# Performance work log

Measured on AMD Instinct MI355X. Metric: run time of the kernel, lower is better.

## Reference

```python
import jax, jax.numpy as jnp
import numpy as np

B, L, D, H = 4, 1024, 1024, 16
HD = D // H
EPS = 1e-5


def _split_heads(x):
    b, l, d = x.shape
    return x.reshape(b, l, H, HD).transpose(0, 2, 1, 3)  # [B,H,L,hd]


def _combine_heads(x):
    b, h, l, hd = x.shape
    return x.transpose(0, 2, 1, 3).reshape(b, l, h * hd)


def _attention(q, k, v):
    scores = jnp.einsum('bhqd,bhkd->bhqk', q, k) / jnp.sqrt(jnp.asarray(HD, q.dtype))
    w = jax.nn.softmax(scores, axis=-1)  # dropout is identity in eval mode
    return jnp.einsum('bhqk,bhkd->bhqd', w, v)


def _layernorm(x, g, b):
    mu = jnp.mean(x, axis=-1, keepdims=True)
    var = jnp.mean(jnp.square(x - mu), axis=-1, keepdims=True)
    return (x - mu) * jax.lax.rsqrt(var + EPS) * g + b


def setup_inputs() -> dict:
    key = jax.random.key(0)
    ks = jax.random.split(key, 20)
    s = 1.0 / np.sqrt(D)
    s2 = 1.0 / np.sqrt(2 * D)
    # weights stored as (in, out): y = x @ W + b
    inp = {
        'h_b': jax.random.normal(ks[0], (B, L, D), jnp.float32),
        'h_p': jax.random.normal(ks[1], (B, L, D), jnp.float32),
        'wq': jax.random.uniform(ks[2], (D, D), jnp.float32, -s, s),
        'bq': jnp.zeros((D,), jnp.float32),
        'wk_sem': jax.random.uniform(ks[3], (D, D), jnp.float32, -s, s),
        'bk_sem': jnp.zeros((D,), jnp.float32),
        'wk_syn': jax.random.uniform(ks[4], (D, D), jnp.float32, -s, s),
        'bk_syn': jnp.zeros((D,), jnp.float32),
        'wv': jax.random.uniform(ks[5], (D, D), jnp.float32, -s, s),
        'bv': jnp.zeros((D,), jnp.float32),
        'g_sem_w': jax.random.uniform(ks[6], (2 * D, D), jnp.float32, -s2, s2),
        'g_sem_b': jnp.zeros((D,), jnp.float32),
        'g_syn_w': jax.random.uniform(ks[7], (2 * D, D), jnp.float32, -s2, s2),
        'g_syn_b': jnp.zeros((D,), jnp.float32),
        'ln_sem_g': jnp.ones((D,), jnp.float32),
        'ln_sem_b': jnp.zeros((D,), jnp.float32),
        'ln_syn_g': jnp.ones((D,), jnp.float32),
        'ln_syn_b': jnp.zeros((D,), jnp.float32),
        'fg1_w': jax.random.uniform(ks[8], (2 * D, D), jnp.float32, -s2, s2),
        'fg1_b': jnp.zeros((D,), jnp.float32),
        'fg2_w': jax.random.uniform(ks[9], (D, 1), jnp.float32, -s, s),
        'fg2_b': jnp.zeros((1,), jnp.float32),
    }
    return inp


def reference(h_b, h_p, wq, bq, wk_sem, bk_sem, wk_syn, bk_syn, wv, bv,
              g_sem_w, g_sem_b, g_syn_w, g_syn_b,
              ln_sem_g, ln_sem_b, ln_syn_g, ln_syn_b,
              fg1_w, fg1_b, fg2_w, fg2_b):
    def cross_attn(a, b, kw, kb):
        q = _split_heads(a @ wq + bq)
        k = _split_heads(b @ kw + kb)
        v = _split_heads(b @ wv + bv)
        return _combine_heads(_attention(q, k, v))

    def gate_fusion(orig, enh, gw, gb):
        gate = jax.nn.sigmoid(jnp.concatenate([orig, enh], axis=-1) @ gw + gb)
        return gate * enh + (1.0 - gate) * orig

    # semantic branch: query=h_b, kv=h_p with syntax K/V projections
    enh_b = cross_attn(h_b, h_p, wk_syn, bk_syn)
    hbp = gate_fusion(h_b, enh_b, g_sem_w, g_sem_b)
    hbp = _layernorm(hbp + h_b, ln_sem_g, ln_sem_b)

    # syntax branch: query=h_p, kv=h_b with semantic K projection (as in source)
    enh_p = cross_attn(h_p, h_b, wk_sem, bk_sem)
    hpp = gate_fusion(h_p, enh_p, g_syn_w, g_syn_b)
    hpp = _layernorm(hpp + h_p, ln_syn_g, ln_syn_b)

    cat = jnp.concatenate([hbp, hpp], axis=-1)
    fw = jax.nn.sigmoid(jax.nn.relu(cat @ fg1_w + fg1_b) @ fg2_w + fg2_b)  # [B,L,1]
    return fw * hbp + (1.0 - fw) * hpp
```

## Files before the change

kernel.cpp:

```cpp
#include <hip/hip_runtime.h>


typedef __bf16 bf16;
typedef __attribute__((ext_vector_type(4))) __bf16 bf16x4;
typedef __attribute__((ext_vector_type(8))) __bf16 bf16x8;
typedef __attribute__((ext_vector_type(4))) float f32x4;

#define MFMA16(a, b, c) __builtin_amdgcn_mfma_f32_16x16x32_bf16((a), (b), (c), 0, 0, 0)
#define EXP2(x) __builtin_amdgcn_exp2f(x)

__device__ inline void async16(const bf16* g, bf16* l) {
  __builtin_amdgcn_global_load_lds(
      (const __attribute__((address_space(1))) unsigned int*)g,
      (__attribute__((address_space(3))) unsigned int*)l, 16, 0, 0);
}

__global__ __launch_bounds__(256) void prep_k(
    const float* __restrict__ wq, const float* __restrict__ wk_sem,
    const float* __restrict__ wk_syn, const float* __restrict__ wv,
    const float* __restrict__ g_sem_w, const float* __restrict__ g_syn_w,
    const float* __restrict__ fg1_w, const float* __restrict__ h_b,
    const float* __restrict__ h_p, bf16* __restrict__ wqT,
    bf16* __restrict__ wkSemT, bf16* __restrict__ wkSynT,
    bf16* __restrict__ wvT, bf16* __restrict__ gSemT,
    bf16* __restrict__ gSynT, bf16* __restrict__ fg1T,
    bf16* __restrict__ hbb, bf16* __restrict__ hpb) {
  int blk = blockIdx.x, tid = threadIdx.x;
  if (blk >= 10240) {
    int idx = blk - 10240;
    const float* in = (idx < 2048) ? h_b : h_p;
    bf16* out = (idx < 2048) ? hbb : hpb;
    size_t base = (size_t)(idx & 2047) * 2048 + tid * 8;
    f32x4 x = *(const f32x4*)(in + base), y = *(const f32x4*)(in + base + 4);
    bf16x8 r;
#pragma unroll
    for (int j = 0; j < 4; j++) { r[j] = (bf16)x[j]; r[4 + j] = (bf16)y[j]; }
    *(bf16x8*)(out + base) = r;
    return;
  }
  __shared__ bf16 t[32][33];
  const float* in;
  bf16* out;
  int R, tile;
  if (blk < 4096) {
    int which = blk >> 10;
    tile = blk & 1023;
    R = 1024;
    in = (which == 0) ? wq : (which == 1) ? wk_sem : (which == 2) ? wk_syn : wv;
    out = (which == 0) ? wqT
          : (which == 1) ? wkSemT : (which == 2) ? wkSynT : wvT;
  } else {
    int b2 = blk - 4096;
    int which = b2 >> 11;
    tile = b2 & 2047;
    R = 2048;
    in = (which == 0) ? g_sem_w : (which == 1) ? g_syn_w : fg1_w;
    out = (which == 0) ? gSemT : (which == 1) ? gSynT : fg1T;
  }
  const int C = 1024;
  int c0 = (tile & 31) * 32, r0 = (tile >> 5) * 32;
  int tx = tid & 31, ty = tid >> 5;
#pragma unroll
  for (int i = 0; i < 32; i += 8)
    t[ty + i][tx] = (bf16)in[(size_t)(r0 + ty + i) * C + c0 + tx];
  __syncthreads();
#pragma unroll
  for (int i = 0; i < 32; i += 8)
    out[(size_t)(c0 + ty + i) * R + r0 + tx] = t[tx][ty + i];
}

__device__ inline void stage128(bf16* Ls, const bf16* src, int r0, int k0,
                                int ldk, int tid) {
#pragma unroll
  for (int i = 0; i < 2; i++) {
    int s = tid + i * 256;
    int row = s >> 2, ch = s & 3;
    async16(src + (size_t)(r0 + row) * ldk + k0 + ch * 8,
            Ls + ((size_t)(i * 256 + (tid & ~63))) * 8);
  }
}
__device__ inline void stage64(bf16* Ls, const bf16* src, int r0, int k0,
                               int ldk, int tid) {
  int row = tid >> 2, ch = tid & 3;
  async16(src + (size_t)(r0 + row) * ldk + k0 + ch * 8,
          Ls + ((size_t)(tid & ~63)) * 8);
}

__global__ __launch_bounds__(256) void proj_gemm(
    const bf16* __restrict__ hbb, const bf16* __restrict__ hpb,
    const bf16* __restrict__ wqT, const bf16* __restrict__ wkSemT,
    const bf16* __restrict__ wkSynT, const bf16* __restrict__ wvT,
    const float* __restrict__ bq, const float* __restrict__ bk_sem,
    const float* __restrict__ bk_syn, const float* __restrict__ bv,
    bf16* __restrict__ q0, bf16* __restrict__ q1, bf16* __restrict__ k0b,
    bf16* __restrict__ k1b, bf16* __restrict__ v0t, bf16* __restrict__ v1t) {
  __shared__ bf16 As[128 * 32];
  __shared__ bf16 Bs[128 * 32];
  int tid = threadIdx.x;
  int m0g = blockIdx.y * 128;
  int half = m0g >= 4096;
  int m0 = m0g & 4095;
  int n0g = blockIdx.x * 128;
  int seg = n0g >> 10, n0 = n0g & 1023;

  const bf16* A = half ? hpb : hbb;
  const bf16* Wt = (seg == 0) ? wqT
                   : (seg == 1) ? (half ? wkSynT : wkSemT) : wvT;
  const float* bias = (seg == 0) ? bq
                      : (seg == 1) ? (half ? bk_syn : bk_sem) : bv;

  int w = tid >> 6, lane = tid & 63, quad = lane >> 4, ln = lane & 15;
  int wm = (w >> 1) * 64, wn = (w & 1) * 64;

  const f32x4 z = {0.f, 0.f, 0.f, 0.f};
  f32x4 acc[4][4];
#pragma unroll
  for (int i = 0; i < 4; i++)
#pragma unroll
    for (int j = 0; j < 4; j++) acc[i][j] = z;

  for (int k0 = 0; k0 < 1024; k0 += 32) {
    __syncthreads();
    stage128(Bs, Wt, n0, k0, 1024, tid);
    stage128(As, A, m0, k0, 1024, tid);
    __syncthreads();
    bf16x8 af[4], bfv[4];
#pragma unroll
    for (int mt = 0; mt < 4; mt++)
      af[mt] = *(bf16x8*)(As + (wm + mt * 16 + ln) * 32 + quad * 8);
#pragma unroll
    for (int nt = 0; nt < 4; nt++)
      bfv[nt] = *(bf16x8*)(Bs + (wn + nt * 16 + ln) * 32 + quad * 8);
#pragma unroll
    for (int mt = 0; mt < 4; mt++)
#pragma unroll
      for (int nt = 0; nt < 4; nt++)
        acc[mt][nt] = MFMA16(af[mt], bfv[nt], acc[mt][nt]);
  }

  if (seg == 2) {
    bf16* vt = half ? v0t : v1t;
#pragma unroll
    for (int nt = 0; nt < 4; nt++) {
      int n = n0 + wn + nt * 16 + ln;
      float bvv = bias[n];
#pragma unroll
      for (int mt = 0; mt < 4; mt++) {
        int mb = m0 + wm + mt * 16 + quad * 4;
        bf16x4 pk;
#pragma unroll
        for (int r = 0; r < 4; r++) pk[r] = (bf16)(acc[mt][nt][r] + bvv);
        *(bf16x4*)(vt + (size_t)n * 4096 + mb) = pk;
      }
    }
    return;
  }
  const float scale = (seg == 0) ? 0.1803368801f : 1.f;
  bf16* out = (seg == 0) ? (half ? q1 : q0) : (half ? k0b : k1b);
#pragma unroll
  for (int nt = 0; nt < 4; nt++) {
    int n = n0 + wn + nt * 16 + ln;
    float bvv = bias[n];
#pragma unroll
    for (int mt = 0; mt < 4; mt++) {
      int mb = m0 + wm + mt * 16 + quad * 4;
#pragma unroll
      for (int r = 0; r < 4; r++)
        out[(size_t)(mb + r) * 1024 + n] =
            (bf16)((acc[mt][nt][r] + bvv) * scale);
    }
  }
}

__global__ __launch_bounds__(256) void gate_gemm(
    const bf16* __restrict__ hbb, const bf16* __restrict__ hpb,
    const float* __restrict__ h_b, const float* __restrict__ h_p,
    const bf16* __restrict__ e0, const bf16* __restrict__ e1,
    const bf16* __restrict__ gSemT, const bf16* __restrict__ gSynT,
    const float* __restrict__ g_sem_b, const float* __restrict__ g_syn_b,
    bf16* __restrict__ ln0, bf16* __restrict__ ln1) {
  __shared__ bf16 As[128 * 32];
  __shared__ bf16 Bs[64 * 32];
  int tid = threadIdx.x;
  int m0g = blockIdx.y * 128;
  int half = m0g >= 4096;
  int m0 = m0g & 4095;
  int n0 = blockIdx.x * 64;

  const bf16* A0 = half ? hpb : hbb;
  const float* O0 = half ? h_p : h_b;
  const bf16* A1 = half ? e1 : e0;
  const bf16* Wt = half ? gSynT : gSemT;
  const float* bias = half ? g_syn_b : g_sem_b;
  bf16* out = half ? ln1 : ln0;

  int w = tid >> 6, lane = tid & 63, quad = lane >> 4, ln = lane & 15;
  int wm = (w >> 1) * 64, wn = (w & 1) * 32;

  const f32x4 z = {0.f, 0.f, 0.f, 0.f};
  f32x4 acc[4][2];
#pragma unroll
  for (int i = 0; i < 4; i++)
#pragma unroll
    for (int j = 0; j < 2; j++) acc[i][j] = z;

  for (int k0 = 0; k0 < 2048; k0 += 32) {
    __syncthreads();
    stage64(Bs, Wt, n0, k0, 2048, tid);
    if (k0 < 1024)
      stage128(As, A0, m0, k0, 1024, tid);
    else
      stage128(As, A1, m0, k0 - 1024, 1024, tid);
    __syncthreads();
    bf16x8 af[4], bfv[2];
#pragma unroll
    for (int mt = 0; mt < 4; mt++)
      af[mt] = *(bf16x8*)(As + (wm + mt * 16 + ln) * 32 + quad * 8);
#pragma unroll
    for (int nt = 0; nt < 2; nt++)
      bfv[nt] = *(bf16x8*)(Bs + (wn + nt * 16 + ln) * 32 + quad * 8);
#pragma unroll
    for (int mt = 0; mt < 4; mt++)
#pragma unroll
      for (int nt = 0; nt < 2; nt++)
        acc[mt][nt] = MFMA16(af[mt], bfv[nt], acc[mt][nt]);
  }

#pragma unroll
  for (int nt = 0; nt < 2; nt++) {
    int n = n0 + wn + nt * 16 + ln;
    float bvv = bias[n];
#pragma unroll
    for (int mt = 0; mt < 4; mt++) {
      int mb = m0 + wm + mt * 16 + quad * 4;
#pragma unroll
      for (int r = 0; r < 4; r++) {
        size_t idx = (size_t)(mb + r) * 1024 + n;
        float v = acc[mt][nt][r] + bvv;
        float e = (float)A1[idx], o = O0[idx];
        float g = 1.f / (1.f + __expf(-v));
        out[idx] = (bf16)(g * e + (1.f - g) * o + o);
      }
    }
  }
}

__global__ __launch_bounds__(256) void fg1_gemm(
    const bf16* __restrict__ A0, const bf16* __restrict__ A1,
    const bf16* __restrict__ Wt, const float* __restrict__ bias,
    bf16* __restrict__ out) {
  __shared__ bf16 As[64 * 32];
  __shared__ bf16 Bs[128 * 32];
  int tid = threadIdx.x;
  int m0 = blockIdx.y * 64, n0 = blockIdx.x * 128;
  int w = tid >> 6, lane = tid & 63, quad = lane >> 4, ln = lane & 15;
  int wm = (w >> 1) * 32, wn = (w & 1) * 64;

  const f32x4 z = {0.f, 0.f, 0.f, 0.f};
  f32x4 acc[2][4];
#pragma unroll
  for (int i = 0; i < 2; i++)
#pragma unroll
    for (int j = 0; j < 4; j++) acc[i][j] = z;

  for (int k0 = 0; k0 < 2048; k0 += 32) {
    __syncthreads();
    stage128(Bs, Wt, n0, k0, 2048, tid);
    if (k0 < 1024)
      stage64(As, A0, m0, k0, 1024, tid);
    else
      stage64(As, A1, m0, k0 - 1024, 1024, tid);
    __syncthreads();
    bf16x8 af[2], bfv[4];
#pragma unroll
    for (int mt = 0; mt < 2; mt++)
      af[mt] = *(bf16x8*)(As + (wm + mt * 16 + ln) * 32 + quad * 8);
#pragma unroll
    for (int nt = 0; nt < 4; nt++)
      bfv[nt] = *(bf16x8*)(Bs + (wn + nt * 16 + ln) * 32 + quad * 8);
#pragma unroll
    for (int mt = 0; mt < 2; mt++)
#pragma unroll
      for (int nt = 0; nt < 4; nt++)
        acc[mt][nt] = MFMA16(af[mt], bfv[nt], acc[mt][nt]);
  }

#pragma unroll
  for (int nt = 0; nt < 4; nt++) {
    int n = n0 + wn + nt * 16 + ln;
    float bvv = bias[n];
#pragma unroll
    for (int mt = 0; mt < 2; mt++) {
      int mb = m0 + wm + mt * 16 + quad * 4;
#pragma unroll
      for (int r = 0; r < 4; r++)
        out[(size_t)(mb + r) * 1024 + n] =
            (bf16)fmaxf(acc[mt][nt][r] + bvv, 0.f);
    }
  }
}

__global__ __launch_bounds__(256) void attn_k(
    const bf16* __restrict__ q0, const bf16* __restrict__ q1,
    const bf16* __restrict__ k0b, const bf16* __restrict__ k1b,
    const bf16* __restrict__ v0t, const bf16* __restrict__ v1t,
    bf16* __restrict__ e0, bf16* __restrict__ e1) {
  int x = blockIdx.x;
  int branch = (x >> 3) & 1;
  int bh = (x & 7) * 8 + ((x >> 4) & 7);
  int qblk = x >> 7;
  int h = bh & 15, b = bh >> 4;
  const bf16* Q = branch ? q1 : q0;
  const bf16* Kp = branch ? k1b : k0b;
  const bf16* Vg = branch ? v1t : v0t;
  bf16* O = branch ? e1 : e0;
  size_t kbase = ((size_t)b * 1024) * 1024 + h * 64;
  size_t vbase = (size_t)h * 64 * 4096 + b * 1024;

  __shared__ bf16 Kt[2][4096];
  __shared__ bf16 Vt[2][4096];
  __shared__ bf16 Pw[4][1024];

  int tid = threadIdx.x, w = tid >> 6, lane = tid & 63;
  int quad = lane >> 4, ln = lane & 15;
  int wq0 = qblk * 64 + w * 16;

  int si = tid;
  int srow0 = (si >> 2) & 63, sh0 = 0, sc0 = si & 3;
  size_t wb0 = (size_t)(tid & ~63) * 8;

  bf16x8 qf0 = *(const bf16x8*)(Q + kbase + (size_t)(wq0 + ln) * 1024 + quad * 8);
  bf16x8 qf1 =
      *(const bf16x8*)(Q + kbase + (size_t)(wq0 + ln) * 1024 + 32 + quad * 8);

  const f32x4 z = {0.f, 0.f, 0.f, 0.f};
  f32x4 oacc[4];
#pragma unroll
  for (int i = 0; i < 4; i++) oacc[i] = z;
  float l_acc = 0.f;

#pragma unroll
  for (int i = 0; i < 2; i++) {
    int s = tid + i * 256;
    size_t wb = (size_t)(i * 256 + (tid & ~63)) * 8;
    async16(Kp + kbase + (size_t)((s >> 2) & 63) * 1024 + (s >> 8) * 32 +
                (s & 3) * 8,
            Kt[0] + wb);
    async16(Vg + vbase + (size_t)((s >> 2) & 63) * 4096 + (s >> 8) * 32 +
                (s & 3) * 8,
            Vt[0] + wb);
  }
  (void)srow0; (void)sh0; (void)sc0; (void)wb0;

  for (int it = 0; it < 16; it++) {
    int cur = it & 1;
    __syncthreads();
    if (it + 1 < 16) {
      int kv1 = (it + 1) * 64;
#pragma unroll
      for (int i = 0; i < 2; i++) {
        int s = tid + i * 256;
        size_t wb = (size_t)(i * 256 + (tid & ~63)) * 8;
        async16(Kp + kbase + (size_t)(kv1 + ((s >> 2) & 63)) * 1024 +
                    (s >> 8) * 32 + (s & 3) * 8,
                Kt[1 - cur] + wb);
        async16(Vg + vbase + (size_t)((s >> 2) & 63) * 4096 + kv1 +
                    (s >> 8) * 32 + (s & 3) * 8,
                Vt[1 - cur] + wb);
      }
    }

#pragma unroll
    for (int nt = 0; nt < 4; nt++) {
      bf16x8 kf0 = *(bf16x8*)(Kt[cur] + (nt * 16 + ln) * 32 + quad * 8);
      bf16x8 kf1 = *(bf16x8*)(Kt[cur] + 2048 + (nt * 16 + ln) * 32 + quad * 8);
      f32x4 a = z;
      a = MFMA16(kf0, qf0, a);
      a = MFMA16(kf1, qf1, a);
      bf16x4 pk;
#pragma unroll
      for (int r = 0; r < 4; r++) {
        float p = EXP2(a[r]);
        l_acc += p;
        pk[r] = (bf16)p;
      }
      *(bf16x4*)(Pw[w] + (nt >> 1) * 512 + ln * 32 + (nt & 1) * 16 + quad * 4) =
          pk;
    }

    bf16x8 pa0 = *(bf16x8*)(Pw[w] + ln * 32 + quad * 8);
    bf16x8 pa1 = *(bf16x8*)(Pw[w] + 512 + ln * 32 + quad * 8);
#pragma unroll
    for (int dt = 0; dt < 4; dt++) {
      bf16x8 vb0 = *(bf16x8*)(Vt[cur] + (dt * 16 + ln) * 32 + quad * 8);
      bf16x8 vb1 = *(bf16x8*)(Vt[cur] + 2048 + (dt * 16 + ln) * 32 + quad * 8);
      oacc[dt] = MFMA16(pa0, vb0, oacc[dt]);
      oacc[dt] = MFMA16(pa1, vb1, oacc[dt]);
    }
  }

  l_acc += __shfl_xor(l_acc, 16, 64);
  l_acc += __shfl_xor(l_acc, 32, 64);
  float l_r[4];
#pragma unroll
  for (int r = 0; r < 4; r++)
    l_r[r] = 1.f / __shfl(l_acc, quad * 4 + r, 16);
#pragma unroll
  for (int dt = 0; dt < 4; dt++)
#pragma unroll
    for (int r = 0; r < 4; r++) {
      int q = wq0 + quad * 4 + r;
      O[kbase + (size_t)q * 1024 + dt * 16 + ln] =
          (bf16)(oacc[dt][r] * l_r[r]);
    }
}

__global__ __launch_bounds__(256) void ln_k(
    const bf16* __restrict__ x0, const bf16* __restrict__ x1,
    const float* __restrict__ g0, const float* __restrict__ b0,
    const float* __restrict__ g1, const float* __restrict__ b1,
    bf16* __restrict__ y0, bf16* __restrict__ y1) {
  int rowg = blockIdx.x, tid = threadIdx.x, c = tid * 4;
  int half = rowg >= 4096;
  int row = rowg & 4095;
  const bf16* x = half ? x1 : x0;
  const float* gg = half ? g1 : g0;
  const float* bb = half ? b1 : b0;
  bf16* y = half ? y1 : y0;

  bf16x4 x4 = *(const bf16x4*)(x + (size_t)row * 1024 + c);
  float v[4], s = 0.f, ss = 0.f;
#pragma unroll
  for (int i = 0; i < 4; i++) {
    v[i] = (float)x4[i];
    s += v[i];
    ss += v[i] * v[i];
  }
#pragma unroll
  for (int o = 32; o > 0; o >>= 1) {
    s += __shfl_down(s, o, 64);
    ss += __shfl_down(ss, o, 64);
  }
  __shared__ float red[8];
  int w = tid >> 6;
  if ((tid & 63) == 0) { red[w] = s; red[4 + w] = ss; }
  __syncthreads();
  s = red[0] + red[1] + red[2] + red[3];
  ss = red[4] + red[5] + red[6] + red[7];
  float mu = s * (1.f / 1024.f);
  float var = ss * (1.f / 1024.f) - mu * mu;
  float rstd = rsqrtf(var + 1e-5f);
  f32x4 g4 = *(const f32x4*)(gg + c), b4 = *(const f32x4*)(bb + c);
  bf16x4 o4;
#pragma unroll
  for (int i = 0; i < 4; i++) o4[i] = (bf16)((v[i] - mu) * rstd * g4[i] + b4[i]);
  *(bf16x4*)(y + (size_t)row * 1024 + c) = o4;
}

__global__ __launch_bounds__(256) void fg2mix_k(const bf16* __restrict__ t,
                                                const float* __restrict__ w2,
                                                const float* __restrict__ b2,
                                                const bf16* __restrict__ hbp,
                                                const bf16* __restrict__ hpp,
                                                float* __restrict__ out) {
  int row = blockIdx.x, tid = threadIdx.x, c = tid * 4;
  bf16x4 t4 = *(const bf16x4*)(t + (size_t)row * 1024 + c);
  f32x4 w4 = *(const f32x4*)(w2 + c);
  float s = 0.f;
#pragma unroll
  for (int i = 0; i < 4; i++) s += (float)t4[i] * w4[i];
#pragma unroll
  for (int o = 32; o > 0; o >>= 1) s += __shfl_down(s, o, 64);
  __shared__ float red[4];
  if ((tid & 63) == 0) red[tid >> 6] = s;
  __syncthreads();
  s = red[0] + red[1] + red[2] + red[3];
  float fw = 1.f / (1.f + __expf(-(s + b2[0])));
  bf16x4 a4 = *(const bf16x4*)(hbp + (size_t)row * 1024 + c);
  bf16x4 p4 = *(const bf16x4*)(hpp + (size_t)row * 1024 + c);
  f32x4 o4;
#pragma unroll
  for (int i = 0; i < 4; i++)
    o4[i] = fw * (float)a4[i] + (1.f - fw) * (float)p4[i];
  *(f32x4*)(out + (size_t)row * 1024 + c) = o4;
}

extern "C" void kernel_launch(void* const* d_in, const int* in_sizes, int n_in,
                              void* d_out, int out_size, void* d_ws,
                              size_t ws_size, hipStream_t stream) {
  const float* h_b     = (const float*)d_in[0];
  const float* h_p     = (const float*)d_in[1];
  const float* wq      = (const float*)d_in[2];
  const float* bq      = (const float*)d_in[3];
  const float* wk_sem  = (const float*)d_in[4];
  const float* bk_sem  = (const float*)d_in[5];
  const float* wk_syn  = (const float*)d_in[6];
  const float* bk_syn  = (const float*)d_in[7];
  const float* wv      = (const float*)d_in[8];
  const float* bv      = (const float*)d_in[9];
  const float* g_sem_w = (const float*)d_in[10];
  const float* g_sem_b = (const float*)d_in[11];
  const float* g_syn_w = (const float*)d_in[12];
  const float* g_syn_b = (const float*)d_in[13];
  const float* ln_sem_g = (const float*)d_in[14];
  const float* ln_sem_b = (const float*)d_in[15];
  const float* ln_syn_g = (const float*)d_in[16];
  const float* ln_syn_b = (const float*)d_in[17];
  const float* fg1_w   = (const float*)d_in[18];
  const float* fg1_b   = (const float*)d_in[19];
  const float* fg2_w   = (const float*)d_in[20];
  const float* fg2_b   = (const float*)d_in[21];

  bf16* ws = (bf16*)d_ws;
  const size_t M1 = 1024ull * 1024ull;
  bf16* wqT    = ws + 0 * M1;
  bf16* wkSemT = ws + 1 * M1;
  bf16* wkSynT = ws + 2 * M1;
  bf16* wvT    = ws + 3 * M1;
  bf16* gSemT  = ws + 4 * M1;
  bf16* gSynT  = ws + 6 * M1;
  bf16* fg1T   = ws + 8 * M1;
  bf16* q0  = ws + 10 * M1;
  bf16* q1  = ws + 14 * M1;
  bf16* k0b = ws + 18 * M1;
  bf16* k1b = ws + 22 * M1;
  bf16* v0t = ws + 26 * M1;
  bf16* v1t = ws + 30 * M1;
  bf16* e0b = ws + 34 * M1;
  bf16* e1b = ws + 38 * M1;
  bf16* hbb = (bf16*)d_out;
  bf16* hpb = hbb + 4 * M1;
  bf16* ln0 = q0;
  bf16* ln1 = q1;
  bf16* hbp = k0b;
  bf16* hpp = k1b;
  bf16* tb  = v0t;

  prep_k<<<14336, 256, 0, stream>>>(wq, wk_sem, wk_syn, wv, g_sem_w, g_syn_w,
                                    fg1_w, h_b, h_p, wqT, wkSemT, wkSynT, wvT,
                                    gSemT, gSynT, fg1T, hbb, hpb);

  proj_gemm<<<dim3(24, 64), 256, 0, stream>>>(
      hbb, hpb, wqT, wkSemT, wkSynT, wvT, bq, bk_sem, bk_syn, bv,
      q0, q1, k0b, k1b, v0t, v1t);

  attn_k<<<2048, 256, 0, stream>>>(q0, q1, k0b, k1b, v0t, v1t, e0b, e1b);

  gate_gemm<<<dim3(16, 64), 256, 0, stream>>>(
      hbb, hpb, h_b, h_p, e0b, e1b, gSemT, gSynT, g_sem_b, g_syn_b, ln0, ln1);

  ln_k<<<8192, 256, 0, stream>>>(ln0, ln1, ln_sem_g, ln_sem_b, ln_syn_g,
                                 ln_syn_b, hbp, hpp);

  fg1_gemm<<<dim3(8, 64), 256, 0, stream>>>(hbp, hpp, fg1T, fg1_b, tb);

  fg2mix_k<<<4096, 256, 0, stream>>>(tb, fg2_w, fg2_b, hbp, hpp,
                                     (float*)d_out);
}
```

Before: 422.8 us.

## XOR-swizzle LDS tiles to avoid bank conflicts and widen gate GEMM tile

Applies an XOR swizzle to the 16-byte chunk index when staging A/B tiles, K/V tiles and the P scratch buffer into LDS, and to the matching fragment reads in every GEMM and the attention kernel. The goal is to remove LDS bank conflicts on the 64-byte-row layout. Separately, the gate GEMM tile is widened from 128x64 to 128x128 so each A tile is reused across more columns, and the grid is halved to match. The wider tile doubles that kernel's accumulator registers and halves its block count, which may cut occupancy.

```diff
diff --git a/kernel.cpp b/kernel.cpp
--- a/kernel.cpp
+++ b/kernel.cpp
@@ -74,14 +74,14 @@
 #pragma unroll
   for (int i = 0; i < 2; i++) {
     int s = tid + i * 256;
-    int row = s >> 2, ch = s & 3;
+    int row = s >> 2, ch = (s & 3) ^ ((s >> 3) & 3);
     async16(src + (size_t)(r0 + row) * ldk + k0 + ch * 8,
             Ls + ((size_t)(i * 256 + (tid & ~63))) * 8);
   }
 }
 __device__ inline void stage64(bf16* Ls, const bf16* src, int r0, int k0,
                                int ldk, int tid) {
-  int row = tid >> 2, ch = tid & 3;
+  int row = tid >> 2, ch = (tid & 3) ^ ((tid >> 3) & 3);
   async16(src + (size_t)(r0 + row) * ldk + k0 + ch * 8,
           Ls + ((size_t)(tid & ~63)) * 8);
 }
@@ -111,6 +111,7 @@
 
   int w = tid >> 6, lane = tid & 63, quad = lane >> 4, ln = lane & 15;
   int wm = (w >> 1) * 64, wn = (w & 1) * 64;
+  int swo = (quad ^ ((ln >> 1) & 3)) * 8;
 
   const f32x4 z = {0.f, 0.f, 0.f, 0.f};
   f32x4 acc[4][4];
@@ -127,10 +128,10 @@
     bf16x8 af[4], bfv[4];
 #pragma unroll
     for (int mt = 0; mt < 4; mt++)
-      af[mt] = *(bf16x8*)(As + (wm + mt * 16 + ln) * 32 + quad * 8);
+      af[mt] = *(bf16x8*)(As + (wm + mt * 16 + ln) * 32 + swo);
 #pragma unroll
     for (int nt = 0; nt < 4; nt++)
-      bfv[nt] = *(bf16x8*)(Bs + (wn + nt * 16 + ln) * 32 + quad * 8);
+      bfv[nt] = *(bf16x8*)(Bs + (wn + nt * 16 + ln) * 32 + swo);
 #pragma unroll
     for (int mt = 0; mt < 4; mt++)
 #pragma unroll
@@ -180,12 +181,12 @@
     const float* __restrict__ g_sem_b, const float* __restrict__ g_syn_b,
     bf16* __restrict__ ln0, bf16* __restrict__ ln1) {
   __shared__ bf16 As[128 * 32];
-  __shared__ bf16 Bs[64 * 32];
+  __shared__ bf16 Bs[128 * 32];
   int tid = threadIdx.x;
   int m0g = blockIdx.y * 128;
   int half = m0g >= 4096;
   int m0 = m0g & 4095;
-  int n0 = blockIdx.x * 64;
+  int n0 = blockIdx.x * 128;
 
   const bf16* A0 = half ? hpb : hbb;
   const float* O0 = half ? h_p : h_b;
@@ -195,39 +196,40 @@
   bf16* out = half ? ln1 : ln0;
 
   int w = tid >> 6, lane = tid & 63, quad = lane >> 4, ln = lane & 15;
-  int wm = (w >> 1) * 64, wn = (w & 1) * 32;
+  int wm = (w >> 1) * 64, wn = (w & 1) * 64;
+  int swo = (quad ^ ((ln >> 1) & 3)) * 8;
 
   const f32x4 z = {0.f, 0.f, 0.f, 0.f};
-  f32x4 acc[4][2];
+  f32x4 acc[4][4];
 #pragma unroll
   for (int i = 0; i < 4; i++)
 #pragma unroll
-    for (int j = 0; j < 2; j++) acc[i][j] = z;
+    for (int j = 0; j < 4; j++) acc[i][j] = z;
 
   for (int k0 = 0; k0 < 2048; k0 += 32) {
     __syncthreads();
-    stage64(Bs, Wt, n0, k0, 2048, tid);
+    stage128(Bs, Wt, n0, k0, 2048, tid);
     if (k0 < 1024)
       stage128(As, A0, m0, k0, 1024, tid);
     else
       stage128(As, A1, m0, k0 - 1024, 1024, tid);
     __syncthreads();
-    bf16x8 af[4], bfv[2];
+    bf16x8 af[4], bfv[4];
 #pragma unroll
     for (int mt = 0; mt < 4; mt++)
-      af[mt] = *(bf16x8*)(As + (wm + mt * 16 + ln) * 32 + quad * 8);
-#pragma unroll
-    for (int nt = 0; nt < 2; nt++)
-      bfv[nt] = *(bf16x8*)(Bs + (wn + nt * 16 + ln) * 32 + quad * 8);
+      af[mt] = *(bf16x8*)(As + (wm + mt * 16 + ln) * 32 + swo);
+#pragma unroll
+    for (int nt = 0; nt < 4; nt++)
+      bfv[nt] = *(bf16x8*)(Bs + (wn + nt * 16 + ln) * 32 + swo);
 #pragma unroll
     for (int mt = 0; mt < 4; mt++)
 #pragma unroll
-      for (int nt = 0; nt < 2; nt++)
+      for (int nt = 0; nt < 4; nt++)
         acc[mt][nt] = MFMA16(af[mt], bfv[nt], acc[mt][nt]);
   }
 
 #pragma unroll
-  for (int nt = 0; nt < 2; nt++) {
+  for (int nt = 0; nt < 4; nt++) {
     int n = n0 + wn + nt * 16 + ln;
     float bvv = bias[n];
 #pragma unroll
@@ -255,6 +257,7 @@
   int m0 = blockIdx.y * 64, n0 = blockIdx.x * 128;
   int w = tid >> 6, lane = tid & 63, quad = lane >> 4, ln = lane & 15;
   int wm = (w >> 1) * 32, wn = (w & 1) * 64;
+  int swo = (quad ^ ((ln >> 1) & 3)) * 8;
 
   const f32x4 z = {0.f, 0.f, 0.f, 0.f};
   f32x4 acc[2][4];
@@ -274,10 +277,10 @@
     bf16x8 af[2], bfv[4];
 #pragma unroll
     for (int mt = 0; mt < 2; mt++)
-      af[mt] = *(bf16x8*)(As + (wm + mt * 16 + ln) * 32 + quad * 8);
+      af[mt] = *(bf16x8*)(As + (wm + mt * 16 + ln) * 32 + swo);
 #pragma unroll
     for (int nt = 0; nt < 4; nt++)
-      bfv[nt] = *(bf16x8*)(Bs + (wn + nt * 16 + ln) * 32 + quad * 8);
+      bfv[nt] = *(bf16x8*)(Bs + (wn + nt * 16 + ln) * 32 + swo);
 #pragma unroll
     for (int mt = 0; mt < 2; mt++)
 #pragma unroll
@@ -324,10 +327,7 @@
   int tid = threadIdx.x, w = tid >> 6, lane = tid & 63;
   int quad = lane >> 4, ln = lane & 15;
   int wq0 = qblk * 64 + w * 16;
-
-  int si = tid;
-  int srow0 = (si >> 2) & 63, sh0 = 0, sc0 = si & 3;
-  size_t wb0 = (size_t)(tid & ~63) * 8;
+  int swo = (quad ^ ((ln >> 1) & 3)) * 8;
 
   bf16x8 qf0 = *(const bf16x8*)(Q + kbase + (size_t)(wq0 + ln) * 1024 + quad * 8);
   bf16x8 qf1 =
@@ -342,15 +342,11 @@
 #pragma unroll
   for (int i = 0; i < 2; i++) {
     int s = tid + i * 256;
+    int row = (s >> 2) & 63, hf = s >> 8, ch = (s & 3) ^ ((s >> 3) & 3);
     size_t wb = (size_t)(i * 256 + (tid & ~63)) * 8;
-    async16(Kp + kbase + (size_t)((s >> 2) & 63) * 1024 + (s >> 8) * 32 +
-                (s & 3) * 8,
-            Kt[0] + wb);
-    async16(Vg + vbase + (size_t)((s >> 2) & 63) * 4096 + (s >> 8) * 32 +
-                (s & 3) * 8,
-            Vt[0] + wb);
-  }
-  (void)srow0; (void)sh0; (void)sc0; (void)wb0;
+    async16(Kp + kbase + (size_t)row * 1024 + hf * 32 + ch * 8, Kt[0] + wb);
+    async16(Vg + vbase + (size_t)row * 4096 + hf * 32 + ch * 8, Vt[0] + wb);
+  }
 
   for (int it = 0; it < 16; it++) {
     int cur = it & 1;
@@ -360,20 +356,19 @@
 #pragma unroll
       for (int i = 0; i < 2; i++) {
         int s = tid + i * 256;
+        int row = (s >> 2) & 63, hf = s >> 8, ch = (s & 3) ^ ((s >> 3) & 3);
         size_t wb = (size_t)(i * 256 + (tid & ~63)) * 8;
-        async16(Kp + kbase + (size_t)(kv1 + ((s >> 2) & 63)) * 1024 +
-                    (s >> 8) * 32 + (s & 3) * 8,
+        async16(Kp + kbase + (size_t)(kv1 + row) * 1024 + hf * 32 + ch * 8,
                 Kt[1 - cur] + wb);
-        async16(Vg + vbase + (size_t)((s >> 2) & 63) * 4096 + kv1 +
-                    (s >> 8) * 32 + (s & 3) * 8,
+        async16(Vg + vbase + (size_t)row * 4096 + kv1 + hf * 32 + ch * 8,
                 Vt[1 - cur] + wb);
       }
     }
 
 #pragma unroll
     for (int nt = 0; nt < 4; nt++) {
-      bf16x8 kf0 = *(bf16x8*)(Kt[cur] + (nt * 16 + ln) * 32 + quad * 8);
-      bf16x8 kf1 = *(bf16x8*)(Kt[cur] + 2048 + (nt * 16 + ln) * 32 + quad * 8);
+      bf16x8 kf0 = *(bf16x8*)(Kt[cur] + (nt * 16 + ln) * 32 + swo);
+      bf16x8 kf1 = *(bf16x8*)(Kt[cur] + 2048 + (nt * 16 + ln) * 32 + swo);
       f32x4 a = z;
       a = MFMA16(kf0, qf0, a);
       a = MFMA16(kf1, qf1, a);
@@ -384,16 +379,17 @@
         l_acc += p;
         pk[r] = (bf16)p;
       }
-      *(bf16x4*)(Pw[w] + (nt >> 1) * 512 + ln * 32 + (nt & 1) * 16 + quad * 4) =
+      int cw = ((nt & 1) * 2 + (quad >> 1)) ^ ((ln >> 1) & 3);
+      *(bf16x4*)(Pw[w] + (nt >> 1) * 512 + ln * 32 + cw * 8 + (quad & 1) * 4) =
           pk;
     }
 
-    bf16x8 pa0 = *(bf16x8*)(Pw[w] + ln * 32 + quad * 8);
-    bf16x8 pa1 = *(bf16x8*)(Pw[w] + 512 + ln * 32 + quad * 8);
+    bf16x8 pa0 = *(bf16x8*)(Pw[w] + ln * 32 + swo);
+    bf16x8 pa1 = *(bf16x8*)(Pw[w] + 512 + ln * 32 + swo);
 #pragma unroll
     for (int dt = 0; dt < 4; dt++) {
-      bf16x8 vb0 = *(bf16x8*)(Vt[cur] + (dt * 16 + ln) * 32 + quad * 8);
-      bf16x8 vb1 = *(bf16x8*)(Vt[cur] + 2048 + (dt * 16 + ln) * 32 + quad * 8);
+      bf16x8 vb0 = *(bf16x8*)(Vt[cur] + (dt * 16 + ln) * 32 + swo);
+      bf16x8 vb1 = *(bf16x8*)(Vt[cur] + 2048 + (dt * 16 + ln) * 32 + swo);
       oacc[dt] = MFMA16(pa0, vb0, oacc[dt]);
       oacc[dt] = MFMA16(pa1, vb1, oacc[dt]);
     }
@@ -546,7 +542,7 @@
 
   attn_k<<<2048, 256, 0, stream>>>(q0, q1, k0b, k1b, v0t, v1t, e0b, e1b);
 
-  gate_gemm<<<dim3(16, 64), 256, 0, stream>>>(
+  gate_gemm<<<dim3(8, 64), 256, 0, stream>>>(
       hbb, hpb, h_b, h_p, e0b, e1b, gSemT, gSynT, g_sem_b, g_syn_b, ln0, ln1);
 
   ln_k<<<8192, 256, 0, stream>>>(ln0, ln1, ln_sem_g, ln_sem_b, ln_syn_g,
```

After: 371.0 us. 1.14x faster.
